# Optimization experiments

Hardware: AMD Instinct MI355X
Metric: run time of the kernel (lower is better)

The kernel has to match this reference:

```python
import jax, jax.numpy as jnp
import numpy as np

N = 4096      # nodes
IN = 512      # in_features
H = 8         # heads
D = 64        # out_features // heads (out % heads == 0)
EDGE_PROB = 0.01


def setup_inputs() -> dict:
    key = jax.random.key(0)
    kx, ka, kw, ko, kd = jax.random.split(key, 5)
    x = jax.random.normal(kx, (N, IN), dtype=jnp.float32)
    # dense binary adjacency with self-loops (original indexes adj[loc, :] as a mask)
    adj = (jax.random.uniform(ka, (N, N)) < EDGE_PROB).astype(jnp.float32)
    adj = jnp.maximum(adj, jnp.eye(N, dtype=jnp.float32))
    # stacked per-head params (original keeps Python lists of equal-sized heads)
    W = jax.random.normal(kw, (H, IN, D), dtype=jnp.float32) * (1.0 / np.sqrt(IN))
    a_origin = jax.random.normal(ko, (H, D), dtype=jnp.float32) * 0.1
    a_dst = jax.random.normal(kd, (H, D), dtype=jnp.float32) * 0.1
    return {"x": x, "adj": adj, "W": W, "a_origin": a_origin, "a_dst": a_dst}


def reference(x, adj, W, a_origin, a_dst):
    # per-head projection: mx[h] = x @ W[h]  -> [H, N, D]
    mx = jnp.einsum('nf,hfd->hnd', x, W)
    # clacAttn: e_ij = exp(mx_i . a_origin + mx_j . a_dst), masked by adj[i,:], row-normalised
    s_i = jnp.einsum('hnd,hd->hn', mx, a_origin)   # source term (row)
    t_j = jnp.einsum('hnd,hd->hn', mx, a_dst)      # dest term (col)
    logits = s_i[:, :, None] + t_j[:, None, :]     # [H, N, N]
    neg_inf = jnp.finfo(logits.dtype).min
    masked = jnp.where(adj[None] > 0, logits, neg_inf)
    attn = jax.nn.softmax(masked, axis=-1)         # == exp/masked-sum of original
    out_h = jnp.einsum('hij,hjd->hid', attn, mx)   # [H, N, D]
    # hstack over heads -> [N, H*D]
    return jnp.transpose(out_h, (1, 0, 2)).reshape(N, H * D)
```

## Files before the change

kernel.cpp:

```cpp
#include <hip/hip_runtime.h>
#include <hip/hip_bf16.h>

#define N_NODES 4096
#define IN_F    512
#define HEADS   8
#define DH      64
#define HD      512

typedef __bf16 bf16x8 __attribute__((ext_vector_type(8)));
typedef float  f32x4  __attribute__((ext_vector_type(4)));

__device__ __forceinline__ float bf_lo(unsigned u) { return __uint_as_float(u << 16); }
__device__ __forceinline__ float bf_hi(unsigned u) { return __uint_as_float(u & 0xffff0000u); }

#define MAXNBR 512
#define JCAP   128
#define KP     72

__global__ __launch_bounds__(256, 2) void kA_gemm_scan(
        const float* __restrict__ X, const float* __restrict__ W,
        const float* __restrict__ a_dst, const float* __restrict__ adj,
        __bf16* __restrict__ C, float* __restrict__ et,
        int* __restrict__ deg, int* __restrict__ jl) {
    __shared__ __bf16 As[2][64][KP];
    __shared__ __bf16 Bs[2][64][KP];
    __shared__ float  ts[2][64];
    __shared__ int    jlist[MAXNBR];
    __shared__ int    cnt;
    int tid = threadIdx.x;
    int bid = blockIdx.x;

    if (bid < 512) {
        int h    = bid & 7;
        int y    = bid >> 3;
        int row0 = y * 64, col0 = h * 64;
        int wave = tid >> 6, lane = tid & 63;
        int wm = wave >> 1, wn = wave & 1;
        int lr = lane & 15, kg = lane >> 4;

        f32x4 acc[2][2] = {};

        int sr = tid >> 3, sc = (tid & 7) * 8;
        const float* aptr0 = X + (size_t)(row0 + sr) * IN_F + sc;
        const float* aptr1 = aptr0 + (size_t)32 * IN_F;
        int dcol = tid & 63, fq = (tid >> 6) * 16;
        const float* wptr = W + ((size_t)h * IN_F + fq) * DH + dcol;

        f32x4 pa00 = *(const f32x4*)aptr0, pa01 = *(const f32x4*)(aptr0 + 4);
        f32x4 pa10 = *(const f32x4*)aptr1, pa11 = *(const f32x4*)(aptr1 + 4);
        float wv[16];
        #pragma unroll
        for (int i = 0; i < 16; ++i) wv[i] = wptr[(size_t)i * DH];

        float ad0 = a_dst[h * DH + wn * 32 + lr];
        float ad1 = a_dst[h * DH + wn * 32 + 16 + lr];

        #pragma unroll
        for (int k = 0; k < IN_F / 64; ++k) {
            int cur = k & 1;
            bf16x8 a0 = { (__bf16)pa00[0], (__bf16)pa00[1], (__bf16)pa00[2], (__bf16)pa00[3],
                          (__bf16)pa01[0], (__bf16)pa01[1], (__bf16)pa01[2], (__bf16)pa01[3] };
            bf16x8 a1 = { (__bf16)pa10[0], (__bf16)pa10[1], (__bf16)pa10[2], (__bf16)pa10[3],
                          (__bf16)pa11[0], (__bf16)pa11[1], (__bf16)pa11[2], (__bf16)pa11[3] };
            bf16x8 b0 = { (__bf16)wv[0],  (__bf16)wv[1],  (__bf16)wv[2],  (__bf16)wv[3],
                          (__bf16)wv[4],  (__bf16)wv[5],  (__bf16)wv[6],  (__bf16)wv[7] };
            bf16x8 b1 = { (__bf16)wv[8],  (__bf16)wv[9],  (__bf16)wv[10], (__bf16)wv[11],
                          (__bf16)wv[12], (__bf16)wv[13], (__bf16)wv[14], (__bf16)wv[15] };
            *(bf16x8*)&As[cur][sr][sc]        = a0;
            *(bf16x8*)&As[cur][sr + 32][sc]   = a1;
            *(bf16x8*)&Bs[cur][dcol][fq]      = b0;
            *(bf16x8*)&Bs[cur][dcol][fq + 8]  = b1;
            if (k + 1 < IN_F / 64) {
                int off = (k + 1) * 64;
                pa00 = *(const f32x4*)(aptr0 + off); pa01 = *(const f32x4*)(aptr0 + off + 4);
                pa10 = *(const f32x4*)(aptr1 + off); pa11 = *(const f32x4*)(aptr1 + off + 4);
                const float* wp = wptr + (size_t)off * DH;
                #pragma unroll
                for (int i = 0; i < 16; ++i) wv[i] = wp[(size_t)i * DH];
            }
            __syncthreads();
            #pragma unroll
            for (int kc = 0; kc < 2; ++kc) {
                bf16x8 af0 = *(const bf16x8*)&As[cur][wm * 32 + lr]     [kc * 32 + kg * 8];
                bf16x8 af1 = *(const bf16x8*)&As[cur][wm * 32 + 16 + lr][kc * 32 + kg * 8];
                bf16x8 bf0 = *(const bf16x8*)&Bs[cur][wn * 32 + lr]     [kc * 32 + kg * 8];
                bf16x8 bf1 = *(const bf16x8*)&Bs[cur][wn * 32 + 16 + lr][kc * 32 + kg * 8];
                acc[0][0] = __builtin_amdgcn_mfma_f32_16x16x32_bf16(af0, bf0, acc[0][0], 0, 0, 0);
                acc[0][1] = __builtin_amdgcn_mfma_f32_16x16x32_bf16(af0, bf1, acc[0][1], 0, 0, 0);
                acc[1][0] = __builtin_amdgcn_mfma_f32_16x16x32_bf16(af1, bf0, acc[1][0], 0, 0, 0);
                acc[1][1] = __builtin_amdgcn_mfma_f32_16x16x32_bf16(af1, bf1, acc[1][1], 0, 0, 0);
            }
        }

        #pragma unroll
        for (int mt = 0; mt < 2; ++mt) {
            #pragma unroll
            for (int nt = 0; nt < 2; ++nt) {
                int col = col0 + wn * 32 + nt * 16 + lr;
                #pragma unroll
                for (int r = 0; r < 4; ++r) {
                    int row = row0 + wm * 32 + mt * 16 + kg * 4 + r;
                    C[(size_t)row * HD + col] = (__bf16)acc[mt][nt][r];
                }
            }
        }
        #pragma unroll
        for (int mt = 0; mt < 2; ++mt) {
            #pragma unroll
            for (int r = 0; r < 4; ++r) {
                float p = ad0 * acc[mt][0][r] + ad1 * acc[mt][1][r];
                p += __shfl_xor(p, 1);
                p += __shfl_xor(p, 2);
                p += __shfl_xor(p, 4);
                p += __shfl_xor(p, 8);
                if (lr == 0) ts[wn][wm * 32 + mt * 16 + kg * 4 + r] = p;
            }
        }
        __syncthreads();
        if (tid < 64) {
            float t = ts[0][tid] + ts[1][tid];
            et[(size_t)(row0 + tid) * HEADS + h] = __expf(t);
        }
    } else {
        int i    = bid - 512;
        int lane = tid & 63;
        if (tid == 0) cnt = 0;

        const uint4* arow = (const uint4*)(adj + (size_t)i * N_NODES);
        uint4 v0 = arow[tid];
        uint4 v1 = arow[256 + tid];
        uint4 v2 = arow[512 + tid];
        uint4 v3 = arow[768 + tid];
        int n = (v0.x != 0) + (v0.y != 0) + (v0.z != 0) + (v0.w != 0)
              + (v1.x != 0) + (v1.y != 0) + (v1.z != 0) + (v1.w != 0)
              + (v2.x != 0) + (v2.y != 0) + (v2.z != 0) + (v2.w != 0)
              + (v3.x != 0) + (v3.y != 0) + (v3.z != 0) + (v3.w != 0);
        __syncthreads();

        int pre = n;
        #pragma unroll
        for (int dlt = 1; dlt < 64; dlt <<= 1) {
            int t = __shfl_up(pre, dlt, 64);
            if (lane >= dlt) pre += t;
        }
        int wtot = __shfl(pre, 63, 64);
        int base = 0;
        if (lane == 63) base = atomicAdd(&cnt, wtot);
        base = __shfl(base, 63, 64);
        if (base + wtot <= MAXNBR) {
            int p_ = base + pre - n;
            int jb = tid * 4;
            if (v0.x) jlist[p_++] = jb;
            if (v0.y) jlist[p_++] = jb + 1;
            if (v0.z) jlist[p_++] = jb + 2;
            if (v0.w) jlist[p_++] = jb + 3;
            jb += 1024;
            if (v1.x) jlist[p_++] = jb;
            if (v1.y) jlist[p_++] = jb + 1;
            if (v1.z) jlist[p_++] = jb + 2;
            if (v1.w) jlist[p_++] = jb + 3;
            jb += 1024;
            if (v2.x) jlist[p_++] = jb;
            if (v2.y) jlist[p_++] = jb + 1;
            if (v2.z) jlist[p_++] = jb + 2;
            if (v2.w) jlist[p_++] = jb + 3;
            jb += 1024;
            if (v3.x) jlist[p_++] = jb;
            if (v3.y) jlist[p_++] = jb + 1;
            if (v3.z) jlist[p_++] = jb + 2;
            if (v3.w) jlist[p_++] = jb + 3;
        }
        __syncthreads();
        int c = cnt;
        if (c > JCAP) c = JCAP;
        for (int t = tid; t < c; t += 256) jl[(size_t)i * JCAP + t] = jlist[t];
        if (tid == 0) deg[i] = c;
    }
}

__global__ __launch_bounds__(256) void kB_gather(const int* __restrict__ deg,
                                                 const int* __restrict__ jl,
                                                 const __bf16* __restrict__ mx,
                                                 const float* __restrict__ et,
                                                 float* __restrict__ out) {
    __shared__ int   jlist[JCAP];
    __shared__ float red[3][32][9];
    int tid = threadIdx.x;
    int bid = blockIdx.x;
    int s   = bid & 1;
    int i   = bid >> 1;
    int w   = tid >> 6, lane = tid & 63;
    int g   = lane >> 5, l5 = lane & 31;

    int c = deg[i];
    if (tid < c) jlist[tid] = jl[(size_t)i * JCAP + tid];
    __syncthreads();

    int h = s * 4 + (l5 >> 3);
    const uint4* mxv = (const uint4*)mx + s * 32 + l5;
    const float* etp = et + h;

    float acc[8] = {0.f,0.f,0.f,0.f,0.f,0.f,0.f,0.f};
    float d = 0.f;

    int  k  = w * 2 + g;
    bool m0 = (k < c);
    float e = 0.f;
    uint4 v = {0u,0u,0u,0u};
    if (m0) { int j = jlist[k]; e = etp[j * HEADS]; v = mxv[(size_t)j * 64]; }

    while (m0) {
        int  kn = k + 8;
        bool n0 = (kn < c);
        float en = 0.f;
        uint4 vn = {0u,0u,0u,0u};
        if (n0) { int j = jlist[kn]; en = etp[j * HEADS]; vn = mxv[(size_t)j * 64]; }
        acc[0] += e * bf_lo(v.x);  acc[1] += e * bf_hi(v.x);
        acc[2] += e * bf_lo(v.y);  acc[3] += e * bf_hi(v.y);
        acc[4] += e * bf_lo(v.z);  acc[5] += e * bf_hi(v.z);
        acc[6] += e * bf_lo(v.w);  acc[7] += e * bf_hi(v.w);
        d += e;
        k = kn; m0 = n0; e = en; v = vn;
    }

    #pragma unroll
    for (int q = 0; q < 8; ++q) acc[q] += __shfl_xor(acc[q], 32);
    d += __shfl_xor(d, 32);

    if (w > 0 && g == 0) {
        #pragma unroll
        for (int q = 0; q < 8; ++q) red[w - 1][l5][q] = acc[q];
        red[w - 1][l5][8] = d;
    }
    __syncthreads();
    if (w == 0 && g == 0) {
        #pragma unroll
        for (int r3 = 0; r3 < 3; ++r3) {
            #pragma unroll
            for (int q = 0; q < 8; ++q) acc[q] += red[r3][l5][q];
            d += red[r3][l5][8];
        }
        float inv = 1.f / d;
        f32x4 o0 = { acc[0] * inv, acc[1] * inv, acc[2] * inv, acc[3] * inv };
        f32x4 o1 = { acc[4] * inv, acc[5] * inv, acc[6] * inv, acc[7] * inv };
        float* orow = out + (size_t)i * HD + s * 256 + l5 * 8;
        *(f32x4*)orow       = o0;
        *(f32x4*)(orow + 4) = o1;
    }
}

extern "C" void kernel_launch(void* const* d_in, const int* in_sizes, int n_in,
                              void* d_out, int out_size, void* d_ws, size_t ws_size,
                              hipStream_t stream) {
    const float* x     = (const float*)d_in[0];
    const float* adj   = (const float*)d_in[1];
    const float* W     = (const float*)d_in[2];
    const float* a_dst = (const float*)d_in[4];
    float* out = (float*)d_out;

    char* ws = (char*)d_ws;
    __bf16* mx  = (__bf16*)ws;
    float*  et  = (float*)(ws + 4194304);
    int*    deg = (int*)  (ws + 4325376);
    int*    jl  = (int*)  (ws + 4341760);

    kA_gemm_scan<<<dim3(512 + N_NODES), dim3(256), 0, stream>>>(x, W, a_dst, adj,
                                                                mx, et, deg, jl);
    kB_gather   <<<dim3(N_NODES * 2),   dim3(256), 0, stream>>>(deg, jl, mx, et, out);
}
```

Before: 127.2 us.

## Fuse GEMM/scan and gather into one persistent kernel with grid barrier

```diff
diff --git a/kernel.cpp b/kernel.cpp
--- a/kernel.cpp
+++ b/kernel.cpp
@@ -16,236 +16,254 @@
 #define MAXNBR 512
 #define JCAP   128
 #define KP     72
-
-__global__ __launch_bounds__(256, 2) void kA_gemm_scan(
+#define GRID   448
+#define NGEMM  256
+#define NSCAN  192
+
+union SharedU {
+    struct { __bf16 As[2][64][KP]; __bf16 Bs[2][64][KP]; } g;
+    struct { int jlist[MAXNBR]; } s;
+    struct { int jlist[JCAP]; float red[3][32][9]; } b;
+};
+
+__global__ __launch_bounds__(256, 2) void mega(
         const float* __restrict__ X, const float* __restrict__ W,
         const float* __restrict__ a_dst, const float* __restrict__ adj,
-        __bf16* __restrict__ C, float* __restrict__ et,
-        int* __restrict__ deg, int* __restrict__ jl) {
-    __shared__ __bf16 As[2][64][KP];
-    __shared__ __bf16 Bs[2][64][KP];
-    __shared__ float  ts[2][64];
-    __shared__ int    jlist[MAXNBR];
-    __shared__ int    cnt;
+        __bf16* __restrict__ mx, float* __restrict__ et,
+        int* __restrict__ deg, int* __restrict__ jl,
+        float* __restrict__ out, int* __restrict__ ctr) {
+    __shared__ SharedU u;
+    __shared__ float ts[2][64];
+    __shared__ int   cnt;
     int tid = threadIdx.x;
     int bid = blockIdx.x;
-
-    if (bid < 512) {
-        int h    = bid & 7;
-        int y    = bid >> 3;
-        int row0 = y * 64, col0 = h * 64;
-        int wave = tid >> 6, lane = tid & 63;
+    int lane = tid & 63;
+
+    if (bid < NGEMM) {
+        int wave = tid >> 6;
         int wm = wave >> 1, wn = wave & 1;
         int lr = lane & 15, kg = lane >> 4;
-
-        f32x4 acc[2][2] = {};
-
-        int sr = tid >> 3, sc = (tid & 7) * 8;
-        const float* aptr0 = X + (size_t)(row0 + sr) * IN_F + sc;
-        const float* aptr1 = aptr0 + (size_t)32 * IN_F;
-        int dcol = tid & 63, fq = (tid >> 6) * 16;
-        const float* wptr = W + ((size_t)h * IN_F + fq) * DH + dcol;
-
-        f32x4 pa00 = *(const f32x4*)aptr0, pa01 = *(const f32x4*)(aptr0 + 4);
-        f32x4 pa10 = *(const f32x4*)aptr1, pa11 = *(const f32x4*)(aptr1 + 4);
-        float wv[16];
-        #pragma unroll
-        for (int i = 0; i < 16; ++i) wv[i] = wptr[(size_t)i * DH];
-
-        float ad0 = a_dst[h * DH + wn * 32 + lr];
-        float ad1 = a_dst[h * DH + wn * 32 + 16 + lr];
-
-        #pragma unroll
-        for (int k = 0; k < IN_F / 64; ++k) {
-            int cur = k & 1;
-            bf16x8 a0 = { (__bf16)pa00[0], (__bf16)pa00[1], (__bf16)pa00[2], (__bf16)pa00[3],
-                          (__bf16)pa01[0], (__bf16)pa01[1], (__bf16)pa01[2], (__bf16)pa01[3] };
-            bf16x8 a1 = { (__bf16)pa10[0], (__bf16)pa10[1], (__bf16)pa10[2], (__bf16)pa10[3],
-                          (__bf16)pa11[0], (__bf16)pa11[1], (__bf16)pa11[2], (__bf16)pa11[3] };
-            bf16x8 b0 = { (__bf16)wv[0],  (__bf16)wv[1],  (__bf16)wv[2],  (__bf16)wv[3],
-                          (__bf16)wv[4],  (__bf16)wv[5],  (__bf16)wv[6],  (__bf16)wv[7] };
-            bf16x8 b1 = { (__bf16)wv[8],  (__bf16)wv[9],  (__bf16)wv[10], (__bf16)wv[11],
-                          (__bf16)wv[12], (__bf16)wv[13], (__bf16)wv[14], (__bf16)wv[15] };
-            *(bf16x8*)&As[cur][sr][sc]        = a0;
-            *(bf16x8*)&As[cur][sr + 32][sc]   = a1;
-            *(bf16x8*)&Bs[cur][dcol][fq]      = b0;
-            *(bf16x8*)&Bs[cur][dcol][fq + 8]  = b1;
-            if (k + 1 < IN_F / 64) {
-                int off = (k + 1) * 64;
-                pa00 = *(const f32x4*)(aptr0 + off); pa01 = *(const f32x4*)(aptr0 + off + 4);
-                pa10 = *(const f32x4*)(aptr1 + off); pa11 = *(const f32x4*)(aptr1 + off + 4);
-                const float* wp = wptr + (size_t)off * DH;
-                #pragma unroll
-                for (int i = 0; i < 16; ++i) wv[i] = wp[(size_t)i * DH];
-            }
-            __syncthreads();
-            #pragma unroll
-            for (int kc = 0; kc < 2; ++kc) {
-                bf16x8 af0 = *(const bf16x8*)&As[cur][wm * 32 + lr]     [kc * 32 + kg * 8];
-                bf16x8 af1 = *(const bf16x8*)&As[cur][wm * 32 + 16 + lr][kc * 32 + kg * 8];
-                bf16x8 bf0 = *(const bf16x8*)&Bs[cur][wn * 32 + lr]     [kc * 32 + kg * 8];
-                bf16x8 bf1 = *(const bf16x8*)&Bs[cur][wn * 32 + 16 + lr][kc * 32 + kg * 8];
-                acc[0][0] = __builtin_amdgcn_mfma_f32_16x16x32_bf16(af0, bf0, acc[0][0], 0, 0, 0);
-                acc[0][1] = __builtin_amdgcn_mfma_f32_16x16x32_bf16(af0, bf1, acc[0][1], 0, 0, 0);
-                acc[1][0] = __builtin_amdgcn_mfma_f32_16x16x32_bf16(af1, bf0, acc[1][0], 0, 0, 0);
-                acc[1][1] = __builtin_amdgcn_mfma_f32_16x16x32_bf16(af1, bf1, acc[1][1], 0, 0, 0);
-            }
-        }
-
-        #pragma unroll
-        for (int mt = 0; mt < 2; ++mt) {
-            #pragma unroll
-            for (int nt = 0; nt < 2; ++nt) {
-                int col = col0 + wn * 32 + nt * 16 + lr;
+        #pragma unroll 1
+        for (int tt = 0; tt < 2; ++tt) {
+            int t = bid + tt * 256;
+            int h = t & 7, y = t >> 3;
+            int row0 = y * 64, col0 = h * 64;
+
+            f32x4 acc[2][2] = {};
+
+            int sr = tid >> 3, sc = (tid & 7) * 8;
+            const float* aptr0 = X + (size_t)(row0 + sr) * IN_F + sc;
+            const float* aptr1 = aptr0 + (size_t)32 * IN_F;
+            int dcol = tid & 63, fq = (tid >> 6) * 16;
+            const float* wptr = W + ((size_t)h * IN_F + fq) * DH + dcol;
+
+            f32x4 pa00 = *(const f32x4*)aptr0, pa01 = *(const f32x4*)(aptr0 + 4);
+            f32x4 pa10 = *(const f32x4*)aptr1, pa11 = *(const f32x4*)(aptr1 + 4);
+            float wv[16];
+            #pragma unroll
+            for (int i = 0; i < 16; ++i) wv[i] = wptr[(size_t)i * DH];
+
+            float ad0 = a_dst[h * DH + wn * 32 + lr];
+            float ad1 = a_dst[h * DH + wn * 32 + 16 + lr];
+
+            #pragma unroll
+            for (int k = 0; k < IN_F / 64; ++k) {
+                int cur = k & 1;
+                bf16x8 a0 = { (__bf16)pa00[0], (__bf16)pa00[1], (__bf16)pa00[2], (__bf16)pa00[3],
+                              (__bf16)pa01[0], (__bf16)pa01[1], (__bf16)pa01[2], (__bf16)pa01[3] };
+                bf16x8 a1 = { (__bf16)pa10[0], (__bf16)pa10[1], (__bf16)pa10[2], (__bf16)pa10[3],
+                              (__bf16)pa11[0], (__bf16)pa11[1], (__bf16)pa11[2], (__bf16)pa11[3] };
+                bf16x8 b0 = { (__bf16)wv[0],  (__bf16)wv[1],  (__bf16)wv[2],  (__bf16)wv[3],
+                              (__bf16)wv[4],  (__bf16)wv[5],  (__bf16)wv[6],  (__bf16)wv[7] };
+                bf16x8 b1 = { (__bf16)wv[8],  (__bf16)wv[9],  (__bf16)wv[10], (__bf16)wv[11],
+                              (__bf16)wv[12], (__bf16)wv[13], (__bf16)wv[14], (__bf16)wv[15] };
+                *(bf16x8*)&u.g.As[cur][sr][sc]       = a0;
+                *(bf16x8*)&u.g.As[cur][sr + 32][sc]  = a1;
+                *(bf16x8*)&u.g.Bs[cur][dcol][fq]     = b0;
+                *(bf16x8*)&u.g.Bs[cur][dcol][fq + 8] = b1;
+                if (k + 1 < IN_F / 64) {
+                    int off = (k + 1) * 64;
+                    pa00 = *(const f32x4*)(aptr0 + off); pa01 = *(const f32x4*)(aptr0 + off + 4);
+                    pa10 = *(const f32x4*)(aptr1 + off); pa11 = *(const f32x4*)(aptr1 + off + 4);
+                    const float* wp = wptr + (size_t)off * DH;
+                    #pragma unroll
+                    for (int i = 0; i < 16; ++i) wv[i] = wp[(size_t)i * DH];
+                }
+                __syncthreads();
+                #pragma unroll
+                for (int kc = 0; kc < 2; ++kc) {
+                    bf16x8 af0 = *(const bf16x8*)&u.g.As[cur][wm * 32 + lr]     [kc * 32 + kg * 8];
+                    bf16x8 af1 = *(const bf16x8*)&u.g.As[cur][wm * 32 + 16 + lr][kc * 32 + kg * 8];
+                    bf16x8 bf0 = *(const bf16x8*)&u.g.Bs[cur][wn * 32 + lr]     [kc * 32 + kg * 8];
+                    bf16x8 bf1 = *(const bf16x8*)&u.g.Bs[cur][wn * 32 + 16 + lr][kc * 32 + kg * 8];
+                    acc[0][0] = __builtin_amdgcn_mfma_f32_16x16x32_bf16(af0, bf0, acc[0][0], 0, 0, 0);
+                    acc[0][1] = __builtin_amdgcn_mfma_f32_16x16x32_bf16(af0, bf1, acc[0][1], 0, 0, 0);
+                    acc[1][0] = __builtin_amdgcn_mfma_f32_16x16x32_bf16(af1, bf0, acc[1][0], 0, 0, 0);
+                    acc[1][1] = __builtin_amdgcn_mfma_f32_16x16x32_bf16(af1, bf1, acc[1][1], 0, 0, 0);
+                }
+            }
+
+            #pragma unroll
+            for (int mt = 0; mt < 2; ++mt) {
+                #pragma unroll
+                for (int nt = 0; nt < 2; ++nt) {
+                    int col = col0 + wn * 32 + nt * 16 + lr;
+                    #pragma unroll
+                    for (int r = 0; r < 4; ++r) {
+                        int row = row0 + wm * 32 + mt * 16 + kg * 4 + r;
+                        mx[(size_t)row * HD + col] = (__bf16)acc[mt][nt][r];
+                    }
+                }
+            }
+            #pragma unroll
+            for (int mt = 0; mt < 2; ++mt) {
                 #pragma unroll
                 for (int r = 0; r < 4; ++r) {
-                    int row = row0 + wm * 32 + mt * 16 + kg * 4 + r;
-                    C[(size_t)row * HD + col] = (__bf16)acc[mt][nt][r];
-                }
-            }
-        }
-        #pragma unroll
-        for (int mt = 0; mt < 2; ++mt) {
-            #pragma unroll
-            for (int r = 0; r < 4; ++r) {
-                float p = ad0 * acc[mt][0][r] + ad1 * acc[mt][1][r];
-                p += __shfl_xor(p, 1);
-                p += __shfl_xor(p, 2);
-                p += __shfl_xor(p, 4);
-                p += __shfl_xor(p, 8);
-                if (lr == 0) ts[wn][wm * 32 + mt * 16 + kg * 4 + r] = p;
-            }
-        }
-        __syncthreads();
-        if (tid < 64) {
-            float t = ts[0][tid] + ts[1][tid];
-            et[(size_t)(row0 + tid) * HEADS + h] = __expf(t);
+                    float p = ad0 * acc[mt][0][r] + ad1 * acc[mt][1][r];
+                    p += __shfl_xor(p, 1);
+                    p += __shfl_xor(p, 2);
+                    p += __shfl_xor(p, 4);
+                    p += __shfl_xor(p, 8);
+                    if (lr == 0) ts[wn][wm * 32 + mt * 16 + kg * 4 + r] = p;
+                }
+            }
+            __syncthreads();
+            if (tid < 64) {
+                float tv = ts[0][tid] + ts[1][tid];
+                et[(size_t)(row0 + tid) * HEADS + h] = __expf(tv);
+            }
         }
     } else {
-        int i    = bid - 512;
-        int lane = tid & 63;
-        if (tid == 0) cnt = 0;
-
-        const uint4* arow = (const uint4*)(adj + (size_t)i * N_NODES);
-        uint4 v0 = arow[tid];
-        uint4 v1 = arow[256 + tid];
-        uint4 v2 = arow[512 + tid];
-        uint4 v3 = arow[768 + tid];
-        int n = (v0.x != 0) + (v0.y != 0) + (v0.z != 0) + (v0.w != 0)
-              + (v1.x != 0) + (v1.y != 0) + (v1.z != 0) + (v1.w != 0)
-              + (v2.x != 0) + (v2.y != 0) + (v2.z != 0) + (v2.w != 0)
-              + (v3.x != 0) + (v3.y != 0) + (v3.z != 0) + (v3.w != 0);
-        __syncthreads();
-
-        int pre = n;
-        #pragma unroll
-        for (int dlt = 1; dlt < 64; dlt <<= 1) {
-            int t = __shfl_up(pre, dlt, 64);
-            if (lane >= dlt) pre += t;
-        }
-        int wtot = __shfl(pre, 63, 64);
-        int base = 0;
-        if (lane == 63) base = atomicAdd(&cnt, wtot);
-        base = __shfl(base, 63, 64);
-        if (base + wtot <= MAXNBR) {
-            int p_ = base + pre - n;
-            int jb = tid * 4;
-            if (v0.x) jlist[p_++] = jb;
-            if (v0.y) jlist[p_++] = jb + 1;
-            if (v0.z) jlist[p_++] = jb + 2;
-            if (v0.w) jlist[p_++] = jb + 3;
-            jb += 1024;
-            if (v1.x) jlist[p_++] = jb;
-            if (v1.y) jlist[p_++] = jb + 1;
-            if (v1.z) jlist[p_++] = jb + 2;
-            if (v1.w) jlist[p_++] = jb + 3;
-            jb += 1024;
-            if (v2.x) jlist[p_++] = jb;
-            if (v2.y) jlist[p_++] = jb + 1;
-            if (v2.z) jlist[p_++] = jb + 2;
-            if (v2.w) jlist[p_++] = jb + 3;
-            jb += 1024;
-            if (v3.x) jlist[p_++] = jb;
-            if (v3.y) jlist[p_++] = jb + 1;
-            if (v3.z) jlist[p_++] = jb + 2;
-            if (v3.w) jlist[p_++] = jb + 3;
-        }
-        __syncthreads();
-        int c = cnt;
-        if (c > JCAP) c = JCAP;
-        for (int t = tid; t < c; t += 256) jl[(size_t)i * JCAP + t] = jlist[t];
-        if (tid == 0) deg[i] = c;
+        #pragma unroll 1
+        for (int i = bid - NGEMM; i < N_NODES; i += NSCAN) {
+            const uint4* arow = (const uint4*)(adj + (size_t)i * N_NODES);
+            uint4 v0 = arow[tid];
+            uint4 v1 = arow[256 + tid];
+            uint4 v2 = arow[512 + tid];
+            uint4 v3 = arow[768 + tid];
+            int n = (v0.x != 0) + (v0.y != 0) + (v0.z != 0) + (v0.w != 0)
+                  + (v1.x != 0) + (v1.y != 0) + (v1.z != 0) + (v1.w != 0)
+                  + (v2.x != 0) + (v2.y != 0) + (v2.z != 0) + (v2.w != 0)
+                  + (v3.x != 0) + (v3.y != 0) + (v3.z != 0) + (v3.w != 0);
+            __syncthreads();
+            if (tid == 0) cnt = 0;
+            __syncthreads();
+
+            int pre = n;
+            #pragma unroll
+            for (int dlt = 1; dlt < 64; dlt <<= 1) {
+                int t = __shfl_up(pre, dlt, 64);
+                if (lane >= dlt) pre += t;
+            }
+            int wtot = __shfl(pre, 63, 64);
+            int base = 0;
+            if (lane == 63) base = atomicAdd(&cnt, wtot);
+            base = __shfl(base, 63, 64);
+            if (base + wtot <= MAXNBR) {
+                int p_ = base + pre - n;
+                int jb = tid * 4;
+                if (v0.x) u.s.jlist[p_++] = jb;
+                if (v0.y) u.s.jlist[p_++] = jb + 1;
+                if (v0.z) u.s.jlist[p_++] = jb + 2;
+                if (v0.w) u.s.jlist[p_++] = jb + 3;
+                jb += 1024;
+                if (v1.x) u.s.jlist[p_++] = jb;
+                if (v1.y) u.s.jlist[p_++] = jb + 1;
+                if (v1.z) u.s.jlist[p_++] = jb + 2;
+                if (v1.w) u.s.jlist[p_++] = jb + 3;
+                jb += 1024;
+                if (v2.x) u.s.jlist[p_++] = jb;
+                if (v2.y) u.s.jlist[p_++] = jb + 1;
+                if (v2.z) u.s.jlist[p_++] = jb + 2;
+                if (v2.w) u.s.jlist[p_++] = jb + 3;
+                jb += 1024;
+                if (v3.x) u.s.jlist[p_++] = jb;
+                if (v3.y) u.s.jlist[p_++] = jb + 1;
+                if (v3.z) u.s.jlist[p_++] = jb + 2;
+                if (v3.w) u.s.jlist[p_++] = jb + 3;
+            }
+            __syncthreads();
+            int c = cnt;
+            if (c > JCAP) c = JCAP;
+            for (int t = tid; t < c; t += 256) jl[(size_t)i * JCAP + t] = u.s.jlist[t];
+            if (tid == 0) deg[i] = c;
+        }
     }
-}
-
-__global__ __launch_bounds__(256) void kB_gather(const int* __restrict__ deg,
-                                                 const int* __restrict__ jl,
-                                                 const __bf16* __restrict__ mx,
-                                                 const float* __restrict__ et,
-                                                 float* __restrict__ out) {
-    __shared__ int   jlist[JCAP];
-    __shared__ float red[3][32][9];
-    int tid = threadIdx.x;
-    int bid = blockIdx.x;
-    int s   = bid & 1;
-    int i   = bid >> 1;
-    int w   = tid >> 6, lane = tid & 63;
-    int g   = lane >> 5, l5 = lane & 31;
-
-    int c = deg[i];
-    if (tid < c) jlist[tid] = jl[(size_t)i * JCAP + tid];
+
+    __threadfence();
     __syncthreads();
-
-    int h = s * 4 + (l5 >> 3);
-    const uint4* mxv = (const uint4*)mx + s * 32 + l5;
-    const float* etp = et + h;
-
-    float acc[8] = {0.f,0.f,0.f,0.f,0.f,0.f,0.f,0.f};
-    float d = 0.f;
-
-    int  k  = w * 2 + g;
-    bool m0 = (k < c);
-    float e = 0.f;
-    uint4 v = {0u,0u,0u,0u};
-    if (m0) { int j = jlist[k]; e = etp[j * HEADS]; v = mxv[(size_t)j * 64]; }
-
-    while (m0) {
-        int  kn = k + 8;
-        bool n0 = (kn < c);
-        float en = 0.f;
-        uint4 vn = {0u,0u,0u,0u};
-        if (n0) { int j = jlist[kn]; en = etp[j * HEADS]; vn = mxv[(size_t)j * 64]; }
-        acc[0] += e * bf_lo(v.x);  acc[1] += e * bf_hi(v.x);
-        acc[2] += e * bf_lo(v.y);  acc[3] += e * bf_hi(v.y);
-        acc[4] += e * bf_lo(v.z);  acc[5] += e * bf_hi(v.z);
-        acc[6] += e * bf_lo(v.w);  acc[7] += e * bf_hi(v.w);
-        d += e;
-        k = kn; m0 = n0; e = en; v = vn;
-    }
-
-    #pragma unroll
-    for (int q = 0; q < 8; ++q) acc[q] += __shfl_xor(acc[q], 32);
-    d += __shfl_xor(d, 32);
-
-    if (w > 0 && g == 0) {
-        #pragma unroll
-        for (int q = 0; q < 8; ++q) red[w - 1][l5][q] = acc[q];
-        red[w - 1][l5][8] = d;
+    if (tid == 0) {
+        atomicAdd(ctr, 1);
+        long guard = 0;
+        while (atomicAdd(ctr, 0) < GRID && guard < 200000000L) ++guard;
     }
     __syncthreads();
-    if (w == 0 && g == 0) {
+    __threadfence();
+
+    int w  = tid >> 6;
+    int g_ = lane >> 5, l5 = lane & 63 & 31;
+    int s  = bid & 1;
+    int hh = s * 4 + (l5 >> 3);
+    const uint4* mxv = (const uint4*)mx + s * 32 + l5;
+    const float* etp = et + hh;
+
+    #pragma unroll 1
+    for (int sid = bid; sid < 2 * N_NODES; sid += GRID) {
+        int i = sid >> 1;
+
+        int c = deg[i];
+        if (c > JCAP) c = JCAP;
+        if (tid < c) u.b.jlist[tid] = jl[(size_t)i * JCAP + tid];
+        __syncthreads();
+
+        float acc[8] = {0.f,0.f,0.f,0.f,0.f,0.f,0.f,0.f};
+        float d = 0.f;
+
+        int  kk = w * 2 + g_;
+        bool m0 = (kk < c), m1 = (kk + 8 < c);
+        float e0 = 0.f, e1 = 0.f;
+        uint4 v0 = {0u,0u,0u,0u}, v1 = {0u,0u,0u,0u};
+        if (m0) { int j = u.b.jlist[kk];     e0 = etp[j * HEADS]; v0 = mxv[(size_t)j * 64]; }
+        if (m1) { int j = u.b.jlist[kk + 8]; e1 = etp[j * HEADS]; v1 = mxv[(size_t)j * 64]; }
+
+        while (m0) {
+            int  kn = kk + 16;
+            bool mn = (kn < c);
+            float en = 0.f;
+            uint4 vn = {0u,0u,0u,0u};
+            if (mn) { int j = u.b.jlist[kn]; en = etp[j * HEADS]; vn = mxv[(size_t)j * 64]; }
+            acc[0] += e0 * bf_lo(v0.x);  acc[1] += e0 * bf_hi(v0.x);
+            acc[2] += e0 * bf_lo(v0.y);  acc[3] += e0 * bf_hi(v0.y);
+            acc[4] += e0 * bf_lo(v0.z);  acc[5] += e0 * bf_hi(v0.z);
+            acc[6] += e0 * bf_lo(v0.w);  acc[7] += e0 * bf_hi(v0.w);
+            d += e0;
+            kk += 8; m0 = m1; e0 = e1; v0 = v1; m1 = mn; e1 = en; v1 = vn;
+        }
+
         #pragma unroll
-        for (int r3 = 0; r3 < 3; ++r3) {
-            #pragma unroll
-            for (int q = 0; q < 8; ++q) acc[q] += red[r3][l5][q];
-            d += red[r3][l5][8];
-        }
-        float inv = 1.f / d;
-        f32x4 o0 = { acc[0] * inv, acc[1] * inv, acc[2] * inv, acc[3] * inv };
-        f32x4 o1 = { acc[4] * inv, acc[5] * inv, acc[6] * inv, acc[7] * inv };
-        float* orow = out + (size_t)i * HD + s * 256 + l5 * 8;
-        *(f32x4*)orow       = o0;
-        *(f32x4*)(orow + 4) = o1;
+        for (int p = 0; p < 8; ++p) acc[p] += __shfl_xor(acc[p], 32);
+        d += __shfl_xor(d, 32);
+
+        if (w > 0 && g_ == 0) {
+            #pragma unroll
+            for (int p = 0; p < 8; ++p) u.b.red[w - 1][l5][p] = acc[p];
+            u.b.red[w - 1][l5][8] = d;
+        }
+        __syncthreads();
+        if (w == 0 && g_ == 0) {
+            #pragma unroll
+            for (int r3 = 0; r3 < 3; ++r3) {
+                #pragma unroll
+                for (int p = 0; p < 8; ++p) acc[p] += u.b.red[r3][l5][p];
+                d += u.b.red[r3][l5][8];
+            }
+            float inv = 1.f / d;
+            f32x4 o0 = { acc[0] * inv, acc[1] * inv, acc[2] * inv, acc[3] * inv };
+            f32x4 o1 = { acc[4] * inv, acc[5] * inv, acc[6] * inv, acc[7] * inv };
+            float* orow = out + (size_t)i * HD + s * 256 + l5 * 8;
+            *(f32x4*)orow       = o0;
+            *(f32x4*)(orow + 4) = o1;
+        }
     }
 }
 
@@ -263,8 +281,9 @@
     float*  et  = (float*)(ws + 4194304);
     int*    deg = (int*)  (ws + 4325376);
     int*    jl  = (int*)  (ws + 4341760);
-
-    kA_gemm_scan<<<dim3(512 + N_NODES), dim3(256), 0, stream>>>(x, W, a_dst, adj,
-                                                                mx, et, deg, jl);
-    kB_gather   <<<dim3(N_NODES * 2),   dim3(256), 0, stream>>>(deg, jl, mx, et, out);
+    int*    ctr = (int*)  (ws + 6438912);
+
+    hipMemsetAsync(ctr, 0, 16, stream);
+    mega<<<dim3(GRID), dim3(256), 0, stream>>>(x, W, a_dst, adj,
+                                               mx, et, deg, jl, out, ctr);
 }
```

New measurement: 269.2 us. +111.6%, slower.
